# Kernel optimization log

Hardware: AMD Instinct MI355X
Metric: run time of the kernel (lower is better)

The kernel has to match this reference:

```python
import jax, jax.numpy as jnp
import numpy as np
from jax import lax

B = 32768
INPUT_SIZE = 42  # 1 rocket_y + 20*(rock_x, rock_y) + 1 speed
H, W = 10, 15    # grid_height, grid_width
OUT = 3


def setup_inputs() -> dict:
    key = jax.random.key(0)
    ks = jax.random.split(key, 8)
    p = lambda k, s: (jax.random.normal(k, s) * 0.05).astype(jnp.float32)
    x = (jax.random.uniform(ks[0], (B, INPUT_SIZE)) * 16.0).astype(jnp.float32)
    return {
        "x": x,
        "conv1_w": p(ks[1], (16, 2, 3, 3)), "conv1_b": jnp.zeros((16,), jnp.float32),
        "conv2_w": p(ks[2], (32, 16, 3, 3)), "conv2_b": jnp.zeros((32,), jnp.float32),
        "fc1_w": p(ks[3], (32 * H * W + 1, 256)), "fc1_b": jnp.zeros((256,), jnp.float32),
        "fc2_w": p(ks[4], (256, 128)), "fc2_b": jnp.zeros((128,), jnp.float32),
        "fc3_w": p(ks[5], (128, OUT)), "fc3_b": jnp.zeros((OUT,), jnp.float32),
    }


def _conv(h, w, b):
    # 3x3, stride 1, padding 1 (SAME), NCHW / OIHW
    return lax.conv_general_dilated(h, w, (1, 1), "SAME",
                                    dimension_numbers=("NCHW", "OIHW", "NCHW")) \
           + b[None, :, None, None]


def _build_grid(x):
    """Vectorized replacement of the per-sample Python scatter loop."""
    bsz = x.shape[0]
    b = jnp.arange(bsz)
    dt = x.dtype
    # rocket channel: grid[i, rocket_y, 1] = 1 if 0 <= rocket_y < H
    ry = x[:, 0].astype(jnp.int32)
    rv = ((ry >= 0) & (ry < H)).astype(dt)
    rocket = jnp.zeros((bsz, H, W), dt).at[b, jnp.clip(ry, 0, H - 1), 1].add(rv)
    # rock channel: pairs (x, y) at columns (1,2),(3,4),...,(39,40)
    kx = x[:, 1:INPUT_SIZE - 1:2].astype(jnp.int32)  # [B, 20]
    ky = x[:, 2:INPUT_SIZE - 1:2].astype(jnp.int32)  # [B, 20]
    kv = ((kx >= 0) & (ky >= 0) & (kx < W) & (ky < H)).astype(dt)
    rock = jnp.zeros((bsz, H, W), dt).at[
        b[:, None], jnp.clip(ky, 0, H - 1), jnp.clip(kx, 0, W - 1)
    ].max(kv)  # set-to-1 semantics (duplicates ok)
    return jnp.stack([rocket, rock], axis=1)  # [B, 2, H, W]


def reference(x, conv1_w, conv1_b, conv2_w, conv2_b,
              fc1_w, fc1_b, fc2_w, fc2_b, fc3_w, fc3_b):
    grid = _build_grid(x)
    h = jax.nn.relu(_conv(grid, conv1_w, conv1_b))
    h = jax.nn.relu(_conv(h, conv2_w, conv2_b))
    h = h.reshape(x.shape[0], -1)                      # NCHW flatten, matches torch .view
    h = jnp.concatenate([h, x[:, -1:]], axis=1)        # append speed
    h = jax.nn.relu(h @ fc1_w + fc1_b)
    h = jax.nn.relu(h @ fc2_w + fc2_b)
    return h @ fc3_w + fc3_b
```

## Files before the change

### kernel.cpp

```cpp
#include <hip/hip_runtime.h>
#include <hip/hip_bf16.h>
#include <stdint.h>

typedef short short8 __attribute__((ext_vector_type(8)));
typedef float f32x4  __attribute__((ext_vector_type(4)));

__device__ __forceinline__ uint16_t f2bf(float f) {
    union { float f; uint32_t u; } v; v.f = f;
    return (uint16_t)((v.u + 0x7FFFu + ((v.u >> 16) & 1u)) >> 16);
}
__device__ __forceinline__ float bf2f(uint16_t h) {
    union { uint32_t u; float f; } v; v.u = ((uint32_t)h) << 16;
    return v.f;
}
__device__ __forceinline__ void gl_lds16(const void* g, void* l) {
    __builtin_amdgcn_global_load_lds(
        (const __attribute__((address_space(1))) unsigned int*)g,
        (__attribute__((address_space(3))) unsigned int*)l, 16, 0, 0);
}

#define NSAMP_TOT 32768
#define H2_PER_S  5120

__global__ void repack_all(const float* __restrict__ f1w, const float* __restrict__ c2w,
                           const float* __restrict__ c1w, const float* __restrict__ f2w,
                           uint16_t* __restrict__ w1pt, uint16_t* __restrict__ w2rt,
                           uint16_t* __restrict__ w1rt, uint16_t* __restrict__ w2bt) {
    int tid = threadIdx.x, b = blockIdx.x;
    if (b < 160) {
        int f_s = b >> 4, cp = b & 15, n = tid;
        __align__(16) uint16_t vals[32];
        #pragma unroll
        for (int o = 0; o < 32; o++) {
            int c = cp * 2 + (o >> 4), pl = o & 15;
            int p = f_s * 16 + pl;
            float v = (p < 150) ? f1w[(size_t)(c * 150 + p) * 256 + n] : 0.f;
            vals[o] = f2bf(v);
        }
        int win = f_s * 8 + (cp >> 1);
        size_t rowbase = (size_t)n * H2_PER_S + win * 64;
        #pragma unroll
        for (int j = 0; j < 4; j++) {
            int qlog = (cp * 4 + j) & 7;
            int qphy = qlog ^ (n & 7);
            *(uint4*)&w1pt[rowbase + qphy * 8] = *(uint4*)&vals[j * 8];
        }
    } else if (b == 160) {
        for (int t = tid; t < 32 * 160; t += 256) {
            int n = t / 160, k = t % 160;
            float v = 0.f;
            if (k < 144) {
                int tap = k >> 4, ci = k & 15, dy = tap / 3, dx = tap % 3;
                v = c2w[((n * 16 + ci) * 3 + dy) * 3 + dx];
            }
            w2rt[t] = f2bf(v);
        }
        for (int t = tid; t < 16 * 32; t += 256) {
            int n = t >> 5, k = t & 31;
            float v = 0.f;
            if (k < 18) {
                int tap = k >> 1, ch = k & 1;
                int dy = (tap * 11) >> 5, dx = tap - dy * 3;
                v = c1w[((n * 2 + ch) * 3 + dy) * 3 + dx];
            }
            w1rt[t] = f2bf(v);
        }
    } else {
        __shared__ float tr2[32][129];
        int kb = b - 161;
        for (int i = tid; i < 32 * 128; i += 256) {
            int kk = i >> 7, n = i & 127;
            tr2[kk][n] = f2w[(size_t)(kb * 32 + kk) * 128 + n];
        }
        __syncthreads();
        int n = tid >> 1, half = tid & 1;
        __align__(16) uint16_t tmp[16];
        #pragma unroll
        for (int q = 0; q < 16; q++) tmp[q] = f2bf(tr2[half * 16 + q][n]);
        *(uint4*)&w2bt[(size_t)n * 256 + kb * 32 + half * 16]     = *(uint4*)&tmp[0];
        *(uint4*)&w2bt[(size_t)n * 256 + kb * 32 + half * 16 + 8] = *(uint4*)&tmp[8];
    }
}

__launch_bounds__(512, 2)
__global__ void k12_fused(const float* __restrict__ x, const uint16_t* __restrict__ w1rt,
                          const float* __restrict__ c1b, const uint16_t* __restrict__ w2rt,
                          const float* __restrict__ c2b, uint16_t* __restrict__ h2, int s0) {
    __shared__ float sx[8 * 42];
    __shared__ __align__(16) uint16_t grd[8 * 204 * 2];
    __shared__ __align__(16) uint16_t h1s[8 * 204 * 16];
    int tid = threadIdx.x;
    int w = tid >> 6, l = tid & 63, lr = l & 15, lk = l >> 4;

    short8 b1f = *(const short8*)&w1rt[lr * 32 + lk * 8];
    short8 bfr[5][2];
    #pragma unroll
    for (int ks = 0; ks < 5; ks++)
        #pragma unroll
        for (int nf = 0; nf < 2; nf++)
            bfr[ks][nf] = *(const short8*)&w2rt[(nf * 16 + lr) * 160 + ks * 32 + lk * 8];
    float cb1r = c1b[lr];
    float cb0 = c2b[lr], cb1 = c2b[16 + lr];

    uint4 z4 = make_uint4(0, 0, 0, 0);
    for (int i = tid; i < 3672; i += 512) {
        if (i < 408) ((uint4*)grd)[i] = z4;
        else         ((uint4*)h1s)[i - 408] = z4;
    }
    int sbase = s0 + blockIdx.x * 8;
    for (int i = tid; i < 8 * 42; i += 512) sx[i] = x[(size_t)(sbase + i / 42) * 42 + (i % 42)];
    __syncthreads();

    if (tid < 160) {
        int sl = tid / 20, r = tid % 20;
        int kx = (int)sx[sl * 42 + 1 + 2 * r];
        int ky = (int)sx[sl * 42 + 2 + 2 * r];
        if (kx >= 0 && kx < 15 && ky >= 0 && ky < 10)
            grd[(sl * 204 + (ky + 1) * 17 + (kx + 1)) * 2 + 1] = 0x3F80;
    } else if (tid < 168) {
        int sl = tid - 160;
        int ry = (int)sx[sl * 42];
        if (ry >= 0 && ry < 10)
            grd[(sl * 204 + (ry + 1) * 17 + 2) * 2 + 0] = 0x3F80;
    }
    __syncthreads();

    for (int f = w; f < 75; f += 8) {
        int rA = f * 16 + lr;
        int sA = rA / 150, pA = rA - sA * 150;
        int y = pA / 15, xx = pA - y * 15;
        int base = sA * 204 + y * 17 + xx;
        union { uint32_t d[4]; short8 s; } au;
        #pragma unroll
        for (int jj = 0; jj < 4; jj++) {
            int t = lk * 4 + jj;
            int valid = t < 9;
            int tc = valid ? t : 0;
            int dy = (tc * 11) >> 5, dx = tc - dy * 3;
            uint32_t v = *(const uint32_t*)&grd[(base + dy * 17 + dx) * 2];
            au.d[jj] = valid ? v : 0u;
        }
        f32x4 acc = {};
        acc = __builtin_amdgcn_mfma_f32_16x16x32_bf16(au.s, b1f, acc, 0, 0, 0);
        #pragma unroll
        for (int j = 0; j < 4; j++) {
            int row = f * 16 + lk * 4 + j;
            int s2 = row / 150, p2 = row - s2 * 150;
            int y2 = p2 / 15, x2 = p2 - y2 * 15;
            float v = acc[j] + cb1r;
            h1s[(s2 * 204 + (y2 + 1) * 17 + (x2 + 1)) * 16 + lr] = f2bf(v > 0.f ? v : 0.f);
        }
    }
    __syncthreads();

    short8 zz = {0, 0, 0, 0, 0, 0, 0, 0};
    for (int f = w; f < 80; f += 8) {
        int s_local = f / 10, f_s = f - s_local * 10;
        int p160 = f_s * 16 + lr;
        int pA = p160 < 150 ? p160 : 0;
        int y = pA / 15, xx = pA - y * 15;
        f32x4 acc0 = {}, acc1 = {};
        #pragma unroll
        for (int ks = 0; ks < 5; ks++) {
            int idx = ks * 4 + lk;
            int idc = idx < 18 ? idx : 0;
            int tap = idc >> 1, half = idc & 1;
            int dy = (tap * 11) >> 5, dx = tap - dy * 3;
            short8 av = *(const short8*)&h1s[((s_local * 204 + (y + dy) * 17 + (xx + dx)) * 16) + half * 8];
            av = idx < 18 ? av : zz;
            acc0 = __builtin_amdgcn_mfma_f32_16x16x32_bf16(av, bfr[ks][0], acc0, 0, 0, 0);
            acc1 = __builtin_amdgcn_mfma_f32_16x16x32_bf16(av, bfr[ks][1], acc1, 0, 0, 0);
        }
        ushort4 v0, v1;
        { float a = acc0[0] + cb0; v0.x = f2bf(a > 0.f ? a : 0.f); }
        { float a = acc0[1] + cb0; v0.y = f2bf(a > 0.f ? a : 0.f); }
        { float a = acc0[2] + cb0; v0.z = f2bf(a > 0.f ? a : 0.f); }
        { float a = acc0[3] + cb0; v0.w = f2bf(a > 0.f ? a : 0.f); }
        { float a = acc1[0] + cb1; v1.x = f2bf(a > 0.f ? a : 0.f); }
        { float a = acc1[1] + cb1; v1.y = f2bf(a > 0.f ? a : 0.f); }
        { float a = acc1[2] + cb1; v1.z = f2bf(a > 0.f ? a : 0.f); }
        { float a = acc1[3] + cb1; v1.w = f2bf(a > 0.f ? a : 0.f); }
        int k0 = f_s * 512 + lr * 16 + lk * 4;
        int k0s = (k0 & ~63) | (((((k0 >> 3) & 7) ^ s_local)) << 3) | (k0 & 7);
        int k1 = k0 + 256;
        int k1s = (k1 & ~63) | (((((k1 >> 3) & 7) ^ s_local)) << 3) | (k1 & 7);
        size_t sb = (size_t)(blockIdx.x * 8 + s_local) * H2_PER_S;
        *(ushort4*)&h2[sb + k0s] = v0;
        *(ushort4*)&h2[sb + k1s] = v1;
    }
}

__launch_bounds__(512)
__global__ void k3_fused(const uint16_t* __restrict__ h2, const uint16_t* __restrict__ w1pt,
                         const float* __restrict__ f1b, const float* __restrict__ f1w,
                         const float* __restrict__ x, const uint16_t* __restrict__ w2bt,
                         const float* __restrict__ f2b, const float* __restrict__ f3w,
                         const float* __restrict__ f3b, float* __restrict__ out, int s0) {
    #define BUF_E (64 * 64 + 256 * 64)
    __shared__ __align__(16) uint16_t uLDS[3 * BUF_E];
    uint16_t* lH = uLDS;
    __shared__ float sbias[256], swl[256], sspeed[64], sb2[128], sw3[384];
    __shared__ float pf[4][64][3];
    int tid = threadIdx.x;
    int bm = blockIdx.x;
    if (tid < 256) { sbias[tid] = f1b[tid]; swl[tid] = f1w[(size_t)4800 * 256 + tid]; }
    else if (tid < 320) sspeed[tid - 256] = x[(size_t)(s0 + bm * 64 + (tid - 256)) * 42 + 41];
    else if (tid < 448) sb2[tid - 320] = f2b[tid - 320];
    for (int i = tid; i < 384; i += 512) sw3[i] = f3w[i];

    int w = tid >> 6, l = tid & 63, lr = l & 15, lk = l >> 4;
    int wm = w >> 2, wn = w & 3;
    const uint16_t* ga = &h2[(size_t)(bm * 64 + (tid >> 3)) * H2_PER_S + (tid & 7) * 8];
    const uint16_t* gb[4];
    #pragma unroll
    for (int i = 0; i < 4; i++) {
        int c2 = tid + i * 512;
        gb[i] = &w1pt[(size_t)(c2 >> 3) * H2_PER_S + (c2 & 7) * 8];
    }
    int saOff = tid * 8;
    int sbOff[4];
    #pragma unroll
    for (int i = 0; i < 4; i++) sbOff[i] = 4096 + (tid + i * 512) * 8;
    int aoff[2][2], boff[4][2];
    #pragma unroll
    for (int ks = 0; ks < 2; ks++) {
        int cl = (ks * 4 + lk);
        #pragma unroll
        for (int mf = 0; mf < 2; mf++)
            aoff[mf][ks] = (wm * 32 + mf * 16 + lr) * 64 + ((cl ^ (lr & 7)) << 3);
        #pragma unroll
        for (int nf = 0; nf < 4; nf++)
            boff[nf][ks] = 4096 + (wn * 64 + nf * 16 + lr) * 64 + ((cl ^ (lr & 7)) << 3);
    }

    uint16_t* bufA = uLDS;
    uint16_t* bufB = uLDS + BUF_E;
    uint16_t* bufC = uLDS + 2 * BUF_E;

    f32x4 acc[2][4] = {};
    gl_lds16(ga, bufA + saOff); ga += 64;
    #pragma unroll
    for (int i = 0; i < 4; i++) { gl_lds16(gb[i], bufA + sbOff[i]); gb[i] += 64; }
    gl_lds16(ga, bufB + saOff); ga += 64;
    #pragma unroll
    for (int i = 0; i < 4; i++) { gl_lds16(gb[i], bufB + sbOff[i]); gb[i] += 64; }

    for (int kt = 0; kt < 80; kt++) {
        if (kt < 78) {
            gl_lds16(ga, bufC + saOff); ga += 64;
            #pragma unroll
            for (int i = 0; i < 4; i++) { gl_lds16(gb[i], bufC + sbOff[i]); gb[i] += 64; }
            asm volatile("s_waitcnt vmcnt(10)" ::: "memory");
        } else if (kt == 78) {
            asm volatile("s_waitcnt vmcnt(5)" ::: "memory");
        } else {
            asm volatile("s_waitcnt vmcnt(0)" ::: "memory");
        }
        __builtin_amdgcn_s_barrier();
        __builtin_amdgcn_sched_barrier(0);
        #pragma unroll
        for (int ks = 0; ks < 2; ks++) {
            short8 a[2], b[4];
            #pragma unroll
            for (int mf = 0; mf < 2; mf++)
                a[mf] = *(const short8*)&bufA[aoff[mf][ks]];
            #pragma unroll
            for (int nf = 0; nf < 4; nf++)
                b[nf] = *(const short8*)&bufA[boff[nf][ks]];
            #pragma unroll
            for (int mf = 0; mf < 2; mf++)
                #pragma unroll
                for (int nf = 0; nf < 4; nf++)
                    acc[mf][nf] = __builtin_amdgcn_mfma_f32_16x16x32_bf16(a[mf], b[nf], acc[mf][nf], 0, 0, 0);
        }
        uint16_t* t = bufA; bufA = bufB; bufB = bufC; bufC = t;
    }
    __syncthreads();
    #pragma unroll
    for (int mf = 0; mf < 2; mf++) {
        #pragma unroll
        for (int j = 0; j < 4; j++) {
            int r = wm * 32 + mf * 16 + lk * 4 + j;
            float sp = sspeed[r];
            #pragma unroll
            for (int nf = 0; nf < 4; nf++) {
                int col = wn * 64 + nf * 16 + lr;
                float v = acc[mf][nf][j] + sbias[col] + sp * swl[col];
                int cc = col >> 3, cl = col & 7;
                lH[r * 256 + ((cc ^ (r & 7)) << 3) + cl] = f2bf(v > 0.f ? v : 0.f);
            }
        }
    }
    __syncthreads();
    f32x4 acc2[2][2] = {};
    #pragma unroll
    for (int ks2 = 0; ks2 < 8; ks2++) {
        short8 a2[2], bv[2];
        #pragma unroll
        for (int mf2 = 0; mf2 < 2; mf2++) {
            int row = wm * 32 + mf2 * 16 + lr;
            int chunk = (ks2 * 4 + lk) ^ (row & 7);
            a2[mf2] = *(const short8*)&lH[row * 256 + chunk * 8];
        }
        #pragma unroll
        for (int nf2 = 0; nf2 < 2; nf2++)
            bv[nf2] = *(const short8*)&w2bt[(size_t)(wn * 32 + nf2 * 16 + lr) * 256 + ks2 * 32 + lk * 8];
        #pragma unroll
        for (int mf2 = 0; mf2 < 2; mf2++)
            #pragma unroll
            for (int nf2 = 0; nf2 < 2; nf2++)
                acc2[mf2][nf2] = __builtin_amdgcn_mfma_f32_16x16x32_bf16(a2[mf2], bv[nf2], acc2[mf2][nf2], 0, 0, 0);
    }
    float p3[2][4][3];
    #pragma unroll
    for (int mf2 = 0; mf2 < 2; mf2++)
        #pragma unroll
        for (int j = 0; j < 4; j++)
            #pragma unroll
            for (int o = 0; o < 3; o++) p3[mf2][j][o] = 0.f;
    #pragma unroll
    for (int mf2 = 0; mf2 < 2; mf2++) {
        #pragma unroll
        for (int nf2 = 0; nf2 < 2; nf2++) {
            int col = wn * 32 + nf2 * 16 + lr;
            float w0 = sw3[col * 3 + 0], w1v = sw3[col * 3 + 1], w2v = sw3[col * 3 + 2];
            #pragma unroll
            for (int j = 0; j < 4; j++) {
                float v = acc2[mf2][nf2][j] + sb2[col];
                v = v > 0.f ? v : 0.f;
                p3[mf2][j][0] += v * w0;
                p3[mf2][j][1] += v * w1v;
                p3[mf2][j][2] += v * w2v;
            }
        }
    }
    #pragma unroll
    for (int off = 1; off < 16; off <<= 1)
        #pragma unroll
        for (int mf2 = 0; mf2 < 2; mf2++)
            #pragma unroll
            for (int j = 0; j < 4; j++)
                #pragma unroll
                for (int o = 0; o < 3; o++)
                    p3[mf2][j][o] += __shfl_xor(p3[mf2][j][o], off);
    if (lr == 0) {
        #pragma unroll
        for (int mf2 = 0; mf2 < 2; mf2++)
            #pragma unroll
            for (int j = 0; j < 4; j++) {
                int r = wm * 32 + mf2 * 16 + lk * 4 + j;
                #pragma unroll
                for (int o = 0; o < 3; o++) pf[wn][r][o] = p3[mf2][j][o];
            }
    }
    __syncthreads();
    if (tid < 192) {
        int r = tid / 3, o = tid - r * 3;
        out[(size_t)(s0 + bm * 64 + r) * 3 + o] =
            pf[0][r][o] + pf[1][r][o] + pf[2][r][o] + pf[3][r][o] + f3b[o];
    }
    #undef BUF_E
}

extern "C" void kernel_launch(void* const* d_in, const int* in_sizes, int n_in,
                              void* d_out, int out_size, void* d_ws, size_t ws_size,
                              hipStream_t stream) {
    const float* x   = (const float*)d_in[0];
    const float* c1w = (const float*)d_in[1];
    const float* c1b = (const float*)d_in[2];
    const float* c2w = (const float*)d_in[3];
    const float* c2b = (const float*)d_in[4];
    const float* f1w = (const float*)d_in[5];
    const float* f1b = (const float*)d_in[6];
    const float* f2w = (const float*)d_in[7];
    const float* f2b = (const float*)d_in[8];
    const float* f3w = (const float*)d_in[9];
    const float* f3b = (const float*)d_in[10];
    float* out = (float*)d_out;

    char* ws = (char*)d_ws;
    uint16_t* w1pt = (uint16_t*)ws;
    uint16_t* w2rt = (uint16_t*)(ws + 2621440);
    uint16_t* w2bt = (uint16_t*)(ws + 2631680);
    uint16_t* w1rt = (uint16_t*)(ws + 2697216);
    size_t base = 2698240;

    int chunk = NSAMP_TOT;
    while (chunk > 128 && base + (size_t)chunk * 10240 > ws_size) chunk >>= 1;
    uint16_t* h2 = (uint16_t*)(ws + base);

    repack_all<<<169, 256, 0, stream>>>(f1w, c2w, c1w, f2w, w1pt, w2rt, w1rt, w2bt);

    for (int s0 = 0; s0 < NSAMP_TOT; s0 += chunk) {
        k12_fused<<<chunk / 8, 512, 0, stream>>>(x, w1rt, c1b, w2rt, c2b, h2, s0);
        k3_fused<<<chunk / 64, 512, 0, stream>>>(h2, w1pt, f1b, f1w, x, w2bt, f2b, f3w, f3b, out, s0);
    }
}
```

Baseline: 264.7 us.

## Map one sample per wave in conv kernel and reorder GEMM pipeline barrier

The fused conv kernel now gives each wave a single sample and loops over its ten 16-row fragments with full unrolling. Per-element divisions are replaced by small LDS lookup tables and hoisted tap offsets, and bf16 conversion uses a packed v_cvt_pk_bf16_f32 instruction. The h1s row stride is padded from 204 to 205 to spread LDS banks. In the FC GEMM kernel the wait and barrier now come before the next tile's global-to-LDS loads are issued. This removes the race on reusing the buffer that other waves may still be reading, while keeping the same prefetch depth.

```diff
diff --git a/kernel.cpp b/kernel.cpp
--- a/kernel.cpp
+++ b/kernel.cpp
@@ -12,6 +12,11 @@
 __device__ __forceinline__ float bf2f(uint16_t h) {
     union { uint32_t u; float f; } v; v.u = ((uint32_t)h) << 16;
     return v.f;
+}
+__device__ __forceinline__ uint32_t pk2bf(float a, float b) {
+    uint32_t r;
+    asm("v_cvt_pk_bf16_f32 %0, %1, %2" : "=v"(r) : "v"(a), "v"(b));
+    return r;
 }
 __device__ __forceinline__ void gl_lds16(const void* g, void* l) {
     __builtin_amdgcn_global_load_lds(
@@ -88,7 +93,9 @@
                           const float* __restrict__ c2b, uint16_t* __restrict__ h2, int s0) {
     __shared__ float sx[8 * 42];
     __shared__ __align__(16) uint16_t grd[8 * 204 * 2];
-    __shared__ __align__(16) uint16_t h1s[8 * 204 * 16];
+    __shared__ __align__(16) uint16_t h1s[8 * 205 * 16];
+    __shared__ uint16_t lutPO[160];
+    __shared__ uint16_t lutST[160];
     int tid = threadIdx.x;
     int w = tid >> 6, l = tid & 63, lr = l & 15, lk = l >> 4;
 
@@ -103,12 +110,19 @@
     float cb0 = c2b[lr], cb1 = c2b[16 + lr];
 
     uint4 z4 = make_uint4(0, 0, 0, 0);
-    for (int i = tid; i < 3672; i += 512) {
-        if (i < 408) ((uint4*)grd)[i] = z4;
-        else         ((uint4*)h1s)[i - 408] = z4;
+    for (int idx = tid; idx < 3688; idx += 512) {
+        if (idx < 408) ((uint4*)grd)[idx] = z4;
+        else           ((uint4*)h1s)[idx - 408] = z4;
     }
     int sbase = s0 + blockIdx.x * 8;
-    for (int i = tid; i < 8 * 42; i += 512) sx[i] = x[(size_t)(sbase + i / 42) * 42 + (i % 42)];
+    if (tid < 336) sx[tid] = x[(size_t)(sbase + tid / 42) * 42 + (tid % 42)];
+    if (tid >= 336 && tid < 496) {
+        int p = tid - 336;
+        int y = p / 15, xx = p - y * 15;
+        int po = y * 17 + xx;
+        lutPO[p] = (p < 150) ? (uint16_t)po : 0;
+        lutST[p] = (p < 150) ? (uint16_t)((po + 18) * 16) : (uint16_t)(204 * 16);
+    }
     __syncthreads();
 
     if (tid < 160) {
@@ -125,68 +139,80 @@
     }
     __syncthreads();
 
-    for (int f = w; f < 75; f += 8) {
-        int rA = f * 16 + lr;
-        int sA = rA / 150, pA = rA - sA * 150;
-        int y = pA / 15, xx = pA - y * 15;
-        int base = sA * 204 + y * 17 + xx;
+    int goff[4]; uint32_t gmask[4];
+    #pragma unroll
+    for (int jj = 0; jj < 4; jj++) {
+        int t = lk * 4 + jj;
+        int tc = t < 9 ? t : 0;
+        int dy = (tc * 11) >> 5, dx = tc - dy * 3;
+        goff[jj] = dy * 17 + dx;
+        gmask[jj] = (t < 9) ? 0xFFFFFFFFu : 0u;
+    }
+    int sbg  = w * 204;
+    int sb16 = w * 205 * 16;
+
+    #pragma unroll
+    for (int f_s = 0; f_s < 10; f_s++) {
+        int p160 = f_s * 16 + lr;
+        int gbase = sbg + lutPO[p160];
         union { uint32_t d[4]; short8 s; } au;
         #pragma unroll
         for (int jj = 0; jj < 4; jj++) {
-            int t = lk * 4 + jj;
-            int valid = t < 9;
-            int tc = valid ? t : 0;
-            int dy = (tc * 11) >> 5, dx = tc - dy * 3;
-            uint32_t v = *(const uint32_t*)&grd[(base + dy * 17 + dx) * 2];
-            au.d[jj] = valid ? v : 0u;
+            uint32_t v = *(const uint32_t*)&grd[(gbase + goff[jj]) * 2];
+            au.d[jj] = v & gmask[jj];
         }
         f32x4 acc = {};
         acc = __builtin_amdgcn_mfma_f32_16x16x32_bf16(au.s, b1f, acc, 0, 0, 0);
         #pragma unroll
-        for (int j = 0; j < 4; j++) {
-            int row = f * 16 + lk * 4 + j;
-            int s2 = row / 150, p2 = row - s2 * 150;
-            int y2 = p2 / 15, x2 = p2 - y2 * 15;
-            float v = acc[j] + cb1r;
-            h1s[(s2 * 204 + (y2 + 1) * 17 + (x2 + 1)) * 16 + lr] = f2bf(v > 0.f ? v : 0.f);
-        }
-    }
-    __syncthreads();
-
-    short8 zz = {0, 0, 0, 0, 0, 0, 0, 0};
-    for (int f = w; f < 80; f += 8) {
-        int s_local = f / 10, f_s = f - s_local * 10;
+        for (int j = 0; j < 4; j += 2) {
+            float v0 = fmaxf(acc[j] + cb1r, 0.f);
+            float v1 = fmaxf(acc[j + 1] + cb1r, 0.f);
+            uint32_t pk = pk2bf(v0, v1);
+            int p2 = f_s * 16 + lk * 4 + j;
+            h1s[sb16 + lutST[p2] + lr]     = (uint16_t)pk;
+            h1s[sb16 + lutST[p2 + 1] + lr] = (uint16_t)(pk >> 16);
+        }
+    }
+    __syncthreads();
+
+    int cdofs[5];
+    #pragma unroll
+    for (int ks = 0; ks < 5; ks++) {
+        int idx = ks * 4 + lk;
+        int idc = idx < 18 ? idx : 0;
+        int tap = idc >> 1, half = idc & 1;
+        int dy = (tap * 11) >> 5, dx = tap - dy * 3;
+        cdofs[ks] = (dy * 17 + dx) * 16 + half * 8;
+    }
+    uint32_t kmask4 = ((16 + lk) < 18) ? 0xFFFFFFFFu : 0u;
+    int k0lo = lr * 16 + lk * 4;
+    int k0s_base = (k0lo & ~63) | ((((k0lo >> 3) & 7) ^ w) << 3) | (k0lo & 7);
+    size_t sbh2 = (size_t)(blockIdx.x * 8 + w) * H2_PER_S;
+
+    #pragma unroll
+    for (int f_s = 0; f_s < 10; f_s++) {
         int p160 = f_s * 16 + lr;
-        int pA = p160 < 150 ? p160 : 0;
-        int y = pA / 15, xx = pA - y * 15;
+        int abase = sb16 + lutPO[p160] * 16;
         f32x4 acc0 = {}, acc1 = {};
         #pragma unroll
         for (int ks = 0; ks < 5; ks++) {
-            int idx = ks * 4 + lk;
-            int idc = idx < 18 ? idx : 0;
-            int tap = idc >> 1, half = idc & 1;
-            int dy = (tap * 11) >> 5, dx = tap - dy * 3;
-            short8 av = *(const short8*)&h1s[((s_local * 204 + (y + dy) * 17 + (xx + dx)) * 16) + half * 8];
-            av = idx < 18 ? av : zz;
+            short8 av = *(const short8*)&h1s[abase + cdofs[ks]];
+            if (ks == 4) {
+                union { short8 s; uint32_t d[4]; } u; u.s = av;
+                #pragma unroll
+                for (int dd = 0; dd < 4; dd++) u.d[dd] &= kmask4;
+                av = u.s;
+            }
             acc0 = __builtin_amdgcn_mfma_f32_16x16x32_bf16(av, bfr[ks][0], acc0, 0, 0, 0);
             acc1 = __builtin_amdgcn_mfma_f32_16x16x32_bf16(av, bfr[ks][1], acc1, 0, 0, 0);
         }
-        ushort4 v0, v1;
-        { float a = acc0[0] + cb0; v0.x = f2bf(a > 0.f ? a : 0.f); }
-        { float a = acc0[1] + cb0; v0.y = f2bf(a > 0.f ? a : 0.f); }
-        { float a = acc0[2] + cb0; v0.z = f2bf(a > 0.f ? a : 0.f); }
-        { float a = acc0[3] + cb0; v0.w = f2bf(a > 0.f ? a : 0.f); }
-        { float a = acc1[0] + cb1; v1.x = f2bf(a > 0.f ? a : 0.f); }
-        { float a = acc1[1] + cb1; v1.y = f2bf(a > 0.f ? a : 0.f); }
-        { float a = acc1[2] + cb1; v1.z = f2bf(a > 0.f ? a : 0.f); }
-        { float a = acc1[3] + cb1; v1.w = f2bf(a > 0.f ? a : 0.f); }
-        int k0 = f_s * 512 + lr * 16 + lk * 4;
-        int k0s = (k0 & ~63) | (((((k0 >> 3) & 7) ^ s_local)) << 3) | (k0 & 7);
-        int k1 = k0 + 256;
-        int k1s = (k1 & ~63) | (((((k1 >> 3) & 7) ^ s_local)) << 3) | (k1 & 7);
-        size_t sb = (size_t)(blockIdx.x * 8 + s_local) * H2_PER_S;
-        *(ushort4*)&h2[sb + k0s] = v0;
-        *(ushort4*)&h2[sb + k1s] = v1;
+        uint32_t p01 = pk2bf(fmaxf(acc0[0] + cb0, 0.f), fmaxf(acc0[1] + cb0, 0.f));
+        uint32_t p23 = pk2bf(fmaxf(acc0[2] + cb0, 0.f), fmaxf(acc0[3] + cb0, 0.f));
+        uint32_t q01 = pk2bf(fmaxf(acc1[0] + cb1, 0.f), fmaxf(acc1[1] + cb1, 0.f));
+        uint32_t q23 = pk2bf(fmaxf(acc1[2] + cb1, 0.f), fmaxf(acc1[3] + cb1, 0.f));
+        int k0s = f_s * 512 + k0s_base;
+        *(uint2*)&h2[sbh2 + k0s]       = make_uint2(p01, p23);
+        *(uint2*)&h2[sbh2 + k0s + 256] = make_uint2(q01, q23);
     }
 }
 
@@ -246,18 +272,15 @@
     for (int i = 0; i < 4; i++) { gl_lds16(gb[i], bufB + sbOff[i]); gb[i] += 64; }
 
     for (int kt = 0; kt < 80; kt++) {
+        if (kt < 79) asm volatile("s_waitcnt vmcnt(5)" ::: "memory");
+        else         asm volatile("s_waitcnt vmcnt(0)" ::: "memory");
+        __builtin_amdgcn_s_barrier();
+        __builtin_amdgcn_sched_barrier(0);
         if (kt < 78) {
             gl_lds16(ga, bufC + saOff); ga += 64;
             #pragma unroll
             for (int i = 0; i < 4; i++) { gl_lds16(gb[i], bufC + sbOff[i]); gb[i] += 64; }
-            asm volatile("s_waitcnt vmcnt(10)" ::: "memory");
-        } else if (kt == 78) {
-            asm volatile("s_waitcnt vmcnt(5)" ::: "memory");
-        } else {
-            asm volatile("s_waitcnt vmcnt(0)" ::: "memory");
-        }
-        __builtin_amdgcn_s_barrier();
-        __builtin_amdgcn_sched_barrier(0);
+        }
         #pragma unroll
         for (int ks = 0; ks < 2; ks++) {
             short8 a[2], b[4];
```

After: 266.6 us. No clear change (+0.7%).
